# Performance work log

Measured on AMD Instinct MI355X. Metric: run time of the kernel, lower is better.

## Reference

```python
import jax, jax.numpy as jnp
import numpy as np

NEG_INF = -1e30


def setup_inputs() -> dict:
    key = jax.random.key(0)
    k1, k2, k3 = jax.random.split(key, 3)
    B, H, HKV, S, D = 2, 16, 4, 2048, 128
    q = jax.random.normal(k1, (B, H, S, D), dtype=jnp.float32)
    k = jax.random.normal(k2, (B, HKV, S, D), dtype=jnp.float32)
    v = jax.random.normal(k3, (B, HKV, S, D), dtype=jnp.float32)
    return {"q": q, "k": k, "v": v}


def reference(q, k, v):
    # Flash attention math (exact, non-tiled reference): causal + sliding-window
    # masked softmax(QK^T * scale) V with GQA head grouping.
    B, H, M, D = q.shape
    _, HKV, N, _ = k.shape
    G = H // HKV  # num_kv_groups
    W = 512       # sliding window size
    scale = 1.0 / jnp.sqrt(jnp.float32(D))

    qg = q.reshape(B, HKV, G, M, D)
    # scores: [B, HKV, G, M, N]
    scores = jnp.einsum("bkgmd,bknd->bkgmn", qg, k) * scale

    i = jnp.arange(M)[:, None]
    j = jnp.arange(N)[None, :]
    # causal: j <= i ; sliding window: only last W keys visible (i - j < W)
    keep = (j <= i) & ((i - j) < W)
    scores = jnp.where(keep[None, None, None], scores, NEG_INF)

    p = jax.nn.softmax(scores.astype(jnp.float32), axis=-1).astype(q.dtype)
    out = jnp.einsum("bkgmn,bknd->bkgmd", p, v)
    return out.reshape(B, H, M, D)
```

## Files before the change

kernel.cpp:

```cpp
#include <hip/hip_runtime.h>
#include <hip/hip_bf16.h>
#include <stdint.h>

#define SEQ 2048
#define HD  128
#define WIN 512
#define NH  16
#define NKV 4
#define BATCH 2

typedef __attribute__((ext_vector_type(8))) short bf16x8;
typedef __attribute__((ext_vector_type(4))) short bf16x4;
typedef __attribute__((ext_vector_type(4))) float f32x4;
typedef __attribute__((ext_vector_type(4))) uint32_t u32x4;
typedef __attribute__((ext_vector_type(2))) uint32_t u32x2;

#define EXP2(x) __builtin_amdgcn_exp2f(x)

#define AS1(p) ((const __attribute__((address_space(1))) uint32_t*)(p))
#define AS3(p) ((__attribute__((address_space(3))) uint32_t*)(p))

__device__ __forceinline__ uint32_t pk2(float a, float b) {
    __hip_bfloat162 h = __float22bfloat162_rn(make_float2(a, b));
    return *reinterpret_cast<uint32_t*>(&h);
}

__global__ __launch_bounds__(256) void prep_kv(
    const float* __restrict__ k,
    const float* __restrict__ v,
    uint16_t* __restrict__ kb,
    uint16_t* __restrict__ vt)
{
    const int tile = blockIdx.x;
    const int kvh  = tile >> 5;
    const int kt   = tile & 31;
    const int t    = threadIdx.x;

    const float* ksrc = k + ((size_t)kvh * SEQ + kt * 64) * HD;
    const float* vsrc = v + ((size_t)kvh * SEQ + kt * 64) * HD;
    uint16_t* kdst = kb + ((size_t)kvh * SEQ + kt * 64) * HD;
    uint16_t* vdst = vt + ((size_t)kvh * 32 + kt) * (size_t)(64 * HD);

    __shared__ uint16_t lv[64][132];

    #pragma unroll
    for (int i = 0; i < 8; ++i) {
        int u = t + i * 256;
        int row = u >> 5, c4 = u & 31;
        float4 f = *reinterpret_cast<const float4*>(vsrc + row * HD + c4 * 4);
        u32x2 w; w.x = pk2(f.x, f.y); w.y = pk2(f.z, f.w);
        *reinterpret_cast<u32x2*>(&lv[row][c4 * 4]) = w;
    }
    #pragma unroll
    for (int i = 0; i < 8; ++i) {
        int u = t + i * 256;
        int row = u >> 5, c4 = u & 31;
        float4 f = *reinterpret_cast<const float4*>(ksrc + row * HD + c4 * 4);
        u32x2 w; w.x = pk2(f.x, f.y); w.y = pk2(f.z, f.w);
        int col = c4 * 4;
        int e = row * HD + ((((col >> 3) ^ (row & 7)) << 3) | (col & 7));
        *reinterpret_cast<u32x2*>(&kdst[e]) = w;
    }
    __syncthreads();
    #pragma unroll
    for (int i = 0; i < 4; ++i) {
        int g = t + i * 256;
        int dim = g >> 3, pg = g & 7;
        uint32_t w[4];
        #pragma unroll
        for (int jj = 0; jj < 4; ++jj) {
            int p0 = pg * 8 + jj * 2;
            int s0 = p0 >> 5, w0 = p0 & 31;
            int key0 = s0 * 32 + ((w0 >> 2) & 1) * 16 + (w0 >> 3) * 4 + (w0 & 3);
            int p1 = p0 + 1;
            int s1 = p1 >> 5, w1 = p1 & 31;
            int key1 = s1 * 32 + ((w1 >> 2) & 1) * 16 + (w1 >> 3) * 4 + (w1 & 3);
            w[jj] = (uint32_t)lv[key0][dim] | ((uint32_t)lv[key1][dim] << 16);
        }
        int e = dim * 64 + ((pg ^ (dim & 7)) << 3);
        u32x4 wv = {w[0], w[1], w[2], w[3]};
        *reinterpret_cast<u32x4*>(&vdst[e]) = wv;
    }
}

__global__ __launch_bounds__(512, 2) void fa_mfma(
    const float* __restrict__ q,
    const uint16_t* __restrict__ kb,
    const uint16_t* __restrict__ vt,
    float* __restrict__ out)
{
    const int tid  = threadIdx.x;
    const int wave = tid >> 6;
    const int lane = tid & 63;
    const int l4   = lane >> 4;
    const int l15  = lane & 15;

    const int bh   = blockIdx.x >> 4;
    const int qblk = blockIdx.x & 15;
    const int q0   = qblk << 7;
    const int hkv  = (bh & (NH - 1)) >> 2;
    const int b    = bh >> 4;

    const int i0   = q0 + wave * 16;

    __shared__ __align__(16) uint16_t lds_k[2][64 * HD];
    __shared__ __align__(16) uint16_t lds_vt[2][64 * HD];

    const float scale2 = 0.08838834764831845f * 1.4426950408889634f;

    const size_t qbase = (size_t)bh * SEQ * HD;
    const uint16_t* kt_base = kb + (size_t)(b * NKV + hkv) * SEQ * HD;
    const uint16_t* vt_base = vt + (size_t)(b * NKV + hkv) * SEQ * HD;

    bf16x8 qf[4];
    {
        const float* qr = q + qbase + (size_t)(i0 + l15) * HD;
        #pragma unroll
        for (int ks = 0; ks < 4; ++ks) {
            const float4* g = reinterpret_cast<const float4*>(qr + ks * 32 + l4 * 8);
            float4 a = g[0], bq = g[1];
            u32x4 t;
            t.x = pk2(a.x * scale2, a.y * scale2);
            t.y = pk2(a.z * scale2, a.w * scale2);
            t.z = pk2(bq.x * scale2, bq.y * scale2);
            t.w = pk2(bq.z * scale2, bq.w * scale2);
            qf[ks] = __builtin_bit_cast(bf16x8, t);
        }
    }

    f32x4 O[8];
    #pragma unroll
    for (int a2 = 0; a2 < 8; ++a2) O[a2] = (f32x4){0.f, 0.f, 0.f, 0.f};
    float mrow = -1e30f;
    float lrow = 0.f;

    const int kt_lo_blk = (q0 >= 512) ? ((q0 - 511) >> 6) : 0;
    const int kt_hi_blk = (q0 + 127) >> 6;
    const int lo_w = (i0 >= 512) ? ((i0 - 511) >> 6) : 0;
    const int hi_w = (i0 + 15) >> 6;

    auto stage = [&](int kt, int pb) {
        const uint16_t* ks = kt_base + (size_t)kt * 64 * HD;
        const uint16_t* vs = vt_base + (size_t)kt * 64 * HD;
        const int ch = wave * 2;
        #pragma unroll
        for (int c = 0; c < 2; ++c) {
            __builtin_amdgcn_global_load_lds(
                AS1(ks + (ch + c) * 512 + lane * 8),
                AS3(&lds_k[pb][(ch + c) * 512]), 16, 0, 0);
            __builtin_amdgcn_global_load_lds(
                AS1(vs + (ch + c) * 512 + lane * 8),
                AS3(&lds_vt[pb][(ch + c) * 512]), 16, 0, 0);
        }
    };

    stage(kt_lo_blk, 0);
    __syncthreads();

    int par = 0;
    for (int kt = kt_lo_blk; kt <= kt_hi_blk; ++kt) {
        if (kt < kt_hi_blk) stage(kt + 1, par ^ 1);

        if (kt >= lo_w && kt <= hi_w) {
            f32x4 sf[4];
            #pragma unroll
            for (int mt = 0; mt < 4; ++mt) sf[mt] = (f32x4){0.f, 0.f, 0.f, 0.f};
            __builtin_amdgcn_s_setprio(1);
            #pragma unroll
            for (int mt = 0; mt < 4; ++mt) {
                const int arow = mt * 16 + l15;
                #pragma unroll
                for (int ks = 0; ks < 4; ++ks) {
                    bf16x8 af = *reinterpret_cast<const bf16x8*>(
                        &lds_k[par][arow * HD + ((((ks * 4 + l4) ^ (arow & 7))) << 3)]);
                    sf[mt] = __builtin_amdgcn_mfma_f32_16x16x32_bf16(
                        af, qf[ks], sf[mt], 0, 0, 0);
                }
            }
            __builtin_amdgcn_s_setprio(0);
            const bool needmask = (kt == hi_w) || (kt == lo_w && i0 > 511);
            if (needmask) {
                const int iq = i0 + l15;
                #pragma unroll
                for (int mt = 0; mt < 4; ++mt) {
                    int jb = kt * 64 + mt * 16 + l4 * 4;
                    #pragma unroll
                    for (int r = 0; r < 4; ++r) {
                        int j = jb + r;
                        if (!((j <= iq) && (iq - j < WIN))) sf[mt][r] = -1e30f;
                    }
                }
            }
            float a0 = fmaxf(fmaxf(sf[0][0], sf[0][1]), fmaxf(sf[0][2], sf[0][3]));
            float a1 = fmaxf(fmaxf(sf[1][0], sf[1][1]), fmaxf(sf[1][2], sf[1][3]));
            float a2 = fmaxf(fmaxf(sf[2][0], sf[2][1]), fmaxf(sf[2][2], sf[2][3]));
            float a3 = fmaxf(fmaxf(sf[3][0], sf[3][1]), fmaxf(sf[3][2], sf[3][3]));
            float tm = fmaxf(fmaxf(a0, a1), fmaxf(a2, a3));
            tm = fmaxf(tm, __shfl_xor(tm, 16, 64));
            tm = fmaxf(tm, __shfl_xor(tm, 32, 64));
            const bool defer = __all(tm <= mrow + 8.0f);
            if (!defer) {
                float mn = fmaxf(mrow, tm);
                float alpha = EXP2(mrow - mn);
                mrow = mn;
                lrow *= alpha;
                #pragma unroll
                for (int r = 0; r < 4; ++r) {
                    float ar = __shfl(alpha, l4 * 4 + r, 64);
                    #pragma unroll
                    for (int nt = 0; nt < 8; ++nt) O[nt][r] *= ar;
                }
            }
            bf16x4 pfrag[4];
            {
                float me = fmaxf(mrow, -1e20f);
                float s[4];
                #pragma unroll
                for (int mt = 0; mt < 4; ++mt) {
                    float p0 = EXP2(sf[mt][0] - me);
                    float p1 = EXP2(sf[mt][1] - me);
                    float p2 = EXP2(sf[mt][2] - me);
                    float p3 = EXP2(sf[mt][3] - me);
                    u32x2 t;
                    t.x = pk2(p0, p1);
                    t.y = pk2(p2, p3);
                    pfrag[mt] = __builtin_bit_cast(bf16x4, t);
                    s[mt] = (p0 + p1) + (p2 + p3);
                }
                float ts = (s[0] + s[1]) + (s[2] + s[3]);
                ts += __shfl_xor(ts, 16, 64);
                ts += __shfl_xor(ts, 32, 64);
                lrow += ts;
            }
            __builtin_amdgcn_s_setprio(1);
            #pragma unroll
            for (int s = 0; s < 2; ++s) {
                bf16x8 pa = __builtin_shufflevector(pfrag[2 * s], pfrag[2 * s + 1],
                                                    0, 1, 2, 3, 4, 5, 6, 7);
                #pragma unroll
                for (int nt = 0; nt < 8; ++nt) {
                    const int vr = nt * 16 + l15;
                    bf16x8 vf = *reinterpret_cast<const bf16x8*>(
                        &lds_vt[par][vr * 64 + ((((s * 4 + l4) ^ (vr & 7))) << 3)]);
                    O[nt] = __builtin_amdgcn_mfma_f32_16x16x32_bf16(pa, vf, O[nt], 0, 0, 0);
                }
            }
            __builtin_amdgcn_s_setprio(0);
        }
        __syncthreads();
        par ^= 1;
    }

    {
        float inv = 1.0f / lrow;
        #pragma unroll
        for (int r = 0; r < 4; ++r) {
            float li = __shfl(inv, l4 * 4 + r, 64);
            int row = i0 + l4 * 4 + r;
            float* orow = out + qbase + (size_t)row * HD;
            #pragma unroll
            for (int nt = 0; nt < 8; ++nt)
                orow[nt * 16 + l15] = O[nt][r] * li;
        }
    }
}

#define KSTR 136
#define VSTR 72
#define VT_ROWS (HD * VSTR + (HD / 4) * 4)
__device__ __forceinline__ int vt_off(int row, int col) {
    return row * VSTR + (row >> 2) * 4 + col;
}

__global__ __launch_bounds__(512, 2)
void fa_mfma_fused(
    const float* __restrict__ q,
    const float* __restrict__ k,
    const float* __restrict__ v,
    float* __restrict__ out)
{
    const int tid  = threadIdx.x;
    const int wave = tid >> 6;
    const int lane = tid & 63;
    const int l4   = lane >> 4;
    const int l15  = lane & 15;

    const int bh   = blockIdx.x >> 4;
    const int qblk = blockIdx.x & 15;
    const int q0   = qblk << 7;
    const int hkv  = (bh & (NH - 1)) >> 2;
    const int b    = bh >> 4;

    const int i0   = q0 + wave * 16;

    __shared__ __align__(16) uint16_t lds_k[2][64 * KSTR];
    __shared__ __align__(16) uint16_t lds_vt[2][VT_ROWS];

    const float scale2 = 0.08838834764831845f * 1.4426950408889634f;

    const size_t qbase  = (size_t)bh * SEQ * HD;
    const size_t kvbase = (size_t)(b * NKV + hkv) * SEQ * HD;

    bf16x8 qf[4];
    {
        const float* qr = q + qbase + (size_t)(i0 + l15) * HD;
        #pragma unroll
        for (int ks = 0; ks < 4; ++ks) {
            const float4* g = reinterpret_cast<const float4*>(qr + ks * 32 + l4 * 8);
            float4 a = g[0], bq = g[1];
            u32x4 t;
            t.x = pk2(a.x * scale2, a.y * scale2);
            t.y = pk2(a.z * scale2, a.w * scale2);
            t.z = pk2(bq.x * scale2, bq.y * scale2);
            t.w = pk2(bq.z * scale2, bq.w * scale2);
            qf[ks] = __builtin_bit_cast(bf16x8, t);
        }
    }

    f32x4 O[8];
    #pragma unroll
    for (int a2 = 0; a2 < 8; ++a2) O[a2] = (f32x4){0.f, 0.f, 0.f, 0.f};
    float mrow = -1e30f;
    float lrow = 0.f;

    const int kt_lo_blk = (q0 >= 512) ? ((q0 - 511) >> 6) : 0;
    const int kt_hi_blk = (q0 + 127) >> 6;
    const int lo_w = (i0 >= 512) ? ((i0 - 511) >> 6) : 0;
    const int hi_w = (i0 + 15) >> 6;

    const int vdg = tid & 31;
    const int vkg = tid >> 5;
    float4 rKa[2], rKb[2], rV[4];

    auto prefetch_k = [&](int kt) {
        const float* kp = k + kvbase + (size_t)kt * 64 * HD;
        #pragma unroll
        for (int it = 0; it < 2; ++it) {
            int flat8 = tid + it * 512, key = flat8 >> 4, ch = flat8 & 15;
            const float4* g = reinterpret_cast<const float4*>(kp + key * HD + ch * 8);
            rKa[it] = g[0]; rKb[it] = g[1];
        }
    };
    auto prefetch_v = [&](int kt) {
        const float* vp = v + kvbase + (size_t)kt * 64 * HD;
        #pragma unroll
        for (int r = 0; r < 4; ++r)
            rV[r] = *reinterpret_cast<const float4*>(vp + (vkg * 4 + r) * HD + vdg * 4);
    };
    auto pack_k = [&](int pb) {
        #pragma unroll
        for (int it = 0; it < 2; ++it) {
            int flat8 = tid + it * 512, key = flat8 >> 4, ch = flat8 & 15;
            uint4 wv;
            wv.x = pk2(rKa[it].x, rKa[it].y);  wv.y = pk2(rKa[it].z, rKa[it].w);
            wv.z = pk2(rKb[it].x, rKb[it].y);  wv.w = pk2(rKb[it].z, rKb[it].w);
            *reinterpret_cast<uint4*>(&lds_k[pb][key * KSTR + ch * 8]) = wv;
        }
    };
    auto pack_v = [&](int pb) {
        const float* rvf = reinterpret_cast<const float*>(rV);
        #pragma unroll
        for (int i = 0; i < 4; ++i) {
            u32x2 wv;
            wv.x = pk2(rvf[0 * 4 + i], rvf[1 * 4 + i]);
            wv.y = pk2(rvf[2 * 4 + i], rvf[3 * 4 + i]);
            *reinterpret_cast<u32x2*>(&lds_vt[pb][vt_off(vdg * 4 + i, vkg * 4)]) = wv;
        }
    };

    prefetch_k(kt_lo_blk);
    prefetch_v(kt_lo_blk);
    pack_k(0);
    pack_v(0);
    __syncthreads();

    int par = 0;
    for (int kt = kt_lo_blk; kt <= kt_hi_blk; ++kt) {
        const bool more = (kt < kt_hi_blk);
        if (more) prefetch_k(kt + 1);

        if (kt >= lo_w && kt <= hi_w) {
            f32x4 sf[4];
            #pragma unroll
            for (int mt = 0; mt < 4; ++mt) sf[mt] = (f32x4){0.f, 0.f, 0.f, 0.f};
            __builtin_amdgcn_s_setprio(1);
            #pragma unroll
            for (int mt = 0; mt < 4; ++mt) {
                #pragma unroll
                for (int ks = 0; ks < 4; ++ks) {
                    bf16x8 af = *reinterpret_cast<const bf16x8*>(
                        &lds_k[par][(mt * 16 + l15) * KSTR + ks * 32 + l4 * 8]);
                    sf[mt] = __builtin_amdgcn_mfma_f32_16x16x32_bf16(
                        af, qf[ks], sf[mt], 0, 0, 0);
                }
            }
            __builtin_amdgcn_s_setprio(0);
            if (more) { pack_k(par ^ 1); prefetch_v(kt + 1); }
            const bool needmask = (kt == hi_w) || (kt == lo_w && i0 > 511);
            if (needmask) {
                const int iq = i0 + l15;
                #pragma unroll
                for (int mt = 0; mt < 4; ++mt) {
                    int jb = kt * 64 + mt * 16 + l4 * 4;
                    #pragma unroll
                    for (int r = 0; r < 4; ++r) {
                        int j = jb + r;
                        if (!((j <= iq) && (iq - j < WIN))) sf[mt][r] = -1e30f;
                    }
                }
            }
            float a0 = fmaxf(fmaxf(sf[0][0], sf[0][1]), fmaxf(sf[0][2], sf[0][3]));
            float a1 = fmaxf(fmaxf(sf[1][0], sf[1][1]), fmaxf(sf[1][2], sf[1][3]));
            float a2 = fmaxf(fmaxf(sf[2][0], sf[2][1]), fmaxf(sf[2][2], sf[2][3]));
            float a3 = fmaxf(fmaxf(sf[3][0], sf[3][1]), fmaxf(sf[3][2], sf[3][3]));
            float tm = fmaxf(fmaxf(a0, a1), fmaxf(a2, a3));
            tm = fmaxf(tm, __shfl_xor(tm, 16, 64));
            tm = fmaxf(tm, __shfl_xor(tm, 32, 64));
            const bool defer = __all(tm <= mrow + 8.0f);
            if (!defer) {
                float mn = fmaxf(mrow, tm);
                float alpha = EXP2(mrow - mn);
                mrow = mn;
                lrow *= alpha;
                #pragma unroll
                for (int r = 0; r < 4; ++r) {
                    float ar = __shfl(alpha, l4 * 4 + r, 64);
                    #pragma unroll
                    for (int nt = 0; nt < 8; ++nt) O[nt][r] *= ar;
                }
            }
            bf16x4 pfrag[4];
            {
                float me = fmaxf(mrow, -1e20f);
                float s[4];
                #pragma unroll
                for (int mt = 0; mt < 4; ++mt) {
                    float p0 = EXP2(sf[mt][0] - me);
                    float p1 = EXP2(sf[mt][1] - me);
                    float p2 = EXP2(sf[mt][2] - me);
                    float p3 = EXP2(sf[mt][3] - me);
                    u32x2 t;
                    t.x = pk2(p0, p1);
                    t.y = pk2(p2, p3);
                    pfrag[mt] = __builtin_bit_cast(bf16x4, t);
                    s[mt] = (p0 + p1) + (p2 + p3);
                }
                float ts = (s[0] + s[1]) + (s[2] + s[3]);
                ts += __shfl_xor(ts, 16, 64);
                ts += __shfl_xor(ts, 32, 64);
                lrow += ts;
            }
            if (more) pack_v(par ^ 1);
            __builtin_amdgcn_s_setprio(1);
            #pragma unroll
            for (int s = 0; s < 2; ++s) {
                bf16x8 pa = __builtin_shufflevector(pfrag[2 * s], pfrag[2 * s + 1],
                                                    0, 1, 2, 3, 4, 5, 6, 7);
                #pragma unroll
                for (int nt = 0; nt < 8; ++nt) {
                    const int vr = nt * 16 + l15;
                    bf16x4 v0 = *reinterpret_cast<const bf16x4*>(
                        &lds_vt[par][vt_off(vr, s * 32 + l4 * 4)]);
                    bf16x4 v1 = *reinterpret_cast<const bf16x4*>(
                        &lds_vt[par][vt_off(vr, s * 32 + 16 + l4 * 4)]);
                    bf16x8 vf = __builtin_shufflevector(v0, v1, 0, 1, 2, 3, 4, 5, 6, 7);
                    O[nt] = __builtin_amdgcn_mfma_f32_16x16x32_bf16(pa, vf, O[nt], 0, 0, 0);
                }
            }
            __builtin_amdgcn_s_setprio(0);
        } else {
            if (more) { prefetch_v(kt + 1); pack_k(par ^ 1); pack_v(par ^ 1); }
        }
        __syncthreads();
        par ^= 1;
    }

    {
        float inv = 1.0f / lrow;
        #pragma unroll
        for (int r = 0; r < 4; ++r) {
            float li = __shfl(inv, l4 * 4 + r, 64);
            int row = i0 + l4 * 4 + r;
            float* orow = out + qbase + (size_t)row * HD;
            #pragma unroll
            for (int nt = 0; nt < 8; ++nt)
                orow[nt * 16 + l15] = O[nt][r] * li;
        }
    }
}

extern "C" void kernel_launch(void* const* d_in, const int* in_sizes, int n_in,
                              void* d_out, int out_size, void* d_ws, size_t ws_size,
                              hipStream_t stream) {
    const float* q = (const float*)d_in[0];
    const float* k = (const float*)d_in[1];
    const float* v = (const float*)d_in[2];
    float* out     = (float*)d_out;

    const size_t kv_elems = (size_t)BATCH * NKV * SEQ * HD;
    const size_t ws_needed = kv_elems * 2u * sizeof(uint16_t);

    if (d_ws != nullptr && ws_size >= ws_needed) {
        uint16_t* kb  = (uint16_t*)d_ws;
        uint16_t* vtw = kb + kv_elems;
        hipLaunchKernelGGL(prep_kv, dim3(BATCH * NKV * (SEQ / 64)), dim3(256), 0,
                           stream, k, v, kb, vtw);
        hipLaunchKernelGGL(fa_mfma, dim3(BATCH * NH * (SEQ / 128)), dim3(512), 0,
                           stream, q, kb, vtw, out);
    } else {
        hipLaunchKernelGGL(fa_mfma_fused, dim3(BATCH * NH * (SEQ / 128)), dim3(512),
                           0, stream, q, k, v, out);
    }
}
```

Baseline: 121.0 us.

## Enlarge attention tiles to 256 queries per block and 128-key KV tiles

After: 127.9 us. 1.06x slower.

```diff
diff --git a/kernel.cpp b/kernel.cpp
--- a/kernel.cpp
+++ b/kernel.cpp
@@ -83,7 +83,8 @@
     }
 }
 
-__global__ __launch_bounds__(512, 2) void fa_mfma(
+__global__ __launch_bounds__(512) __attribute__((amdgpu_waves_per_eu(2, 2)))
+void fa_mfma(
     const float* __restrict__ q,
     const uint16_t* __restrict__ kb,
     const uint16_t* __restrict__ vt,
@@ -95,6 +96,214 @@
     const int l4   = lane >> 4;
     const int l15  = lane & 15;
 
+    const int bh   = blockIdx.x >> 3;
+    const int qblk = blockIdx.x & 7;
+    const int q0   = qblk << 8;
+    const int hkv  = (bh & (NH - 1)) >> 2;
+    const int b    = bh >> 4;
+
+    const int i0   = q0 + wave * 32;
+
+    __shared__ __align__(16) uint16_t lds_k[2][128 * HD];
+    __shared__ __align__(16) uint16_t lds_vt[2][128 * HD];
+
+    const float scale2 = 0.08838834764831845f * 1.4426950408889634f;
+
+    const size_t qbase = (size_t)bh * SEQ * HD;
+    const uint16_t* kt_base = kb + (size_t)(b * NKV + hkv) * SEQ * HD;
+    const uint16_t* vt_base = vt + (size_t)(b * NKV + hkv) * SEQ * HD;
+
+    bf16x8 qf[2][4];
+    #pragma unroll
+    for (int sub = 0; sub < 2; ++sub) {
+        const float* qr = q + qbase + (size_t)(i0 + sub * 16 + l15) * HD;
+        #pragma unroll
+        for (int ks = 0; ks < 4; ++ks) {
+            const float4* g = reinterpret_cast<const float4*>(qr + ks * 32 + l4 * 8);
+            float4 a = g[0], bq = g[1];
+            u32x4 t;
+            t.x = pk2(a.x * scale2, a.y * scale2);
+            t.y = pk2(a.z * scale2, a.w * scale2);
+            t.z = pk2(bq.x * scale2, bq.y * scale2);
+            t.w = pk2(bq.z * scale2, bq.w * scale2);
+            qf[sub][ks] = __builtin_bit_cast(bf16x8, t);
+        }
+    }
+
+    f32x4 O[2][8];
+    #pragma unroll
+    for (int a1 = 0; a1 < 2; ++a1)
+        #pragma unroll
+        for (int a2 = 0; a2 < 8; ++a2) O[a1][a2] = (f32x4){0.f, 0.f, 0.f, 0.f};
+    float mrow[2] = {-1e30f, -1e30f};
+    float lrow[2] = {0.f, 0.f};
+
+    const int kt_lo_blk = (q0 >= 512) ? ((q0 - 511) >> 7) : 0;
+    const int kt_hi_blk = (q0 + 255) >> 7;
+    const int lo_w = (i0 >= 512) ? ((i0 - 511) >> 7) : 0;
+    const int hi_w = (i0 + 31) >> 7;
+
+    auto stage = [&](int kt, int pb) {
+        const uint16_t* ks = kt_base + (size_t)kt * 128 * HD;
+        const uint16_t* vs = vt_base + (size_t)kt * 128 * HD;
+        #pragma unroll
+        for (int c = 0; c < 4; ++c) {
+            const int off = c * 4096 + tid * 8;
+            __builtin_amdgcn_global_load_lds(AS1(ks + off), AS3(&lds_k[pb][off]),
+                                             16, 0, 0);
+            __builtin_amdgcn_global_load_lds(AS1(vs + off), AS3(&lds_vt[pb][off]),
+                                             16, 0, 0);
+        }
+    };
+
+    stage(kt_lo_blk, 0);
+    __syncthreads();
+
+    int par = 0;
+    for (int kt = kt_lo_blk; kt <= kt_hi_blk; ++kt) {
+        if (kt < kt_hi_blk) stage(kt + 1, par ^ 1);
+
+        if (kt >= lo_w && kt <= hi_w) {
+            f32x4 sf[2][8];
+            #pragma unroll
+            for (int sub = 0; sub < 2; ++sub)
+                #pragma unroll
+                for (int mt = 0; mt < 8; ++mt) sf[sub][mt] = (f32x4){0.f, 0.f, 0.f, 0.f};
+            __builtin_amdgcn_s_setprio(1);
+            #pragma unroll
+            for (int mt = 0; mt < 8; ++mt) {
+                const int arow = mt * 16 + l15;
+                #pragma unroll
+                for (int ks = 0; ks < 4; ++ks) {
+                    bf16x8 af = *reinterpret_cast<const bf16x8*>(
+                        &lds_k[par][arow * HD + ((((ks * 4 + l4) ^ (arow & 7))) << 3)]);
+                    sf[0][mt] = __builtin_amdgcn_mfma_f32_16x16x32_bf16(
+                        af, qf[0][ks], sf[0][mt], 0, 0, 0);
+                    sf[1][mt] = __builtin_amdgcn_mfma_f32_16x16x32_bf16(
+                        af, qf[1][ks], sf[1][mt], 0, 0, 0);
+                }
+            }
+            __builtin_amdgcn_s_setprio(0);
+            const bool needmask = (kt == hi_w) || (kt == lo_w && i0 >= 512);
+            if (needmask) {
+                #pragma unroll
+                for (int sub = 0; sub < 2; ++sub) {
+                    const int iq = i0 + sub * 16 + l15;
+                    #pragma unroll
+                    for (int mt = 0; mt < 8; ++mt) {
+                        int jb = kt * 128 + mt * 16 + l4 * 4;
+                        #pragma unroll
+                        for (int r = 0; r < 4; ++r) {
+                            int j = jb + r;
+                            if (!((j <= iq) && (iq - j < WIN))) sf[sub][mt][r] = -1e30f;
+                        }
+                    }
+                }
+            }
+            bf16x4 pfrag[2][8];
+            #pragma unroll
+            for (int sub = 0; sub < 2; ++sub) {
+                float tmx = -1e30f;
+                #pragma unroll
+                for (int mt = 0; mt < 8; ++mt) {
+                    float a = fmaxf(fmaxf(sf[sub][mt][0], sf[sub][mt][1]),
+                                    fmaxf(sf[sub][mt][2], sf[sub][mt][3]));
+                    tmx = fmaxf(tmx, a);
+                }
+                tmx = fmaxf(tmx, __shfl_xor(tmx, 16, 64));
+                tmx = fmaxf(tmx, __shfl_xor(tmx, 32, 64));
+                const bool defer = __all(tmx <= mrow[sub] + 8.0f);
+                if (!defer) {
+                    float mn = fmaxf(mrow[sub], tmx);
+                    float alpha = EXP2(mrow[sub] - mn);
+                    mrow[sub] = mn;
+                    lrow[sub] *= alpha;
+                    #pragma unroll
+                    for (int r = 0; r < 4; ++r) {
+                        float ar = __shfl(alpha, l4 * 4 + r, 64);
+                        #pragma unroll
+                        for (int nt = 0; nt < 8; ++nt) O[sub][nt][r] *= ar;
+                    }
+                }
+                float me = fmaxf(mrow[sub], -1e20f);
+                float ts = 0.f;
+                #pragma unroll
+                for (int mt = 0; mt < 8; ++mt) {
+                    float p0 = EXP2(sf[sub][mt][0] - me);
+                    float p1 = EXP2(sf[sub][mt][1] - me);
+                    float p2 = EXP2(sf[sub][mt][2] - me);
+                    float p3 = EXP2(sf[sub][mt][3] - me);
+                    u32x2 t;
+                    t.x = pk2(p0, p1);
+                    t.y = pk2(p2, p3);
+                    pfrag[sub][mt] = __builtin_bit_cast(bf16x4, t);
+                    ts += (p0 + p1) + (p2 + p3);
+                }
+                ts += __shfl_xor(ts, 16, 64);
+                ts += __shfl_xor(ts, 32, 64);
+                lrow[sub] += ts;
+            }
+            __builtin_amdgcn_s_setprio(1);
+            #pragma unroll
+            for (int s = 0; s < 4; ++s) {
+                const int st = s >> 1, s2 = s & 1;
+                bf16x8 pa0 = __builtin_shufflevector(pfrag[0][2 * s], pfrag[0][2 * s + 1],
+                                                     0, 1, 2, 3, 4, 5, 6, 7);
+                bf16x8 pa1 = __builtin_shufflevector(pfrag[1][2 * s], pfrag[1][2 * s + 1],
+                                                     0, 1, 2, 3, 4, 5, 6, 7);
+                #pragma unroll
+                for (int nt = 0; nt < 8; ++nt) {
+                    const int vr = nt * 16 + l15;
+                    bf16x8 vf = *reinterpret_cast<const bf16x8*>(
+                        &lds_vt[par][st * 8192 + vr * 64 +
+                                     ((((s2 * 4 + l4) ^ (vr & 7))) << 3)]);
+                    O[0][nt] = __builtin_amdgcn_mfma_f32_16x16x32_bf16(
+                        pa0, vf, O[0][nt], 0, 0, 0);
+                    O[1][nt] = __builtin_amdgcn_mfma_f32_16x16x32_bf16(
+                        pa1, vf, O[1][nt], 0, 0, 0);
+                }
+            }
+            __builtin_amdgcn_s_setprio(0);
+        }
+        __syncthreads();
+        par ^= 1;
+    }
+
+    #pragma unroll
+    for (int sub = 0; sub < 2; ++sub) {
+        float inv = 1.0f / lrow[sub];
+        #pragma unroll
+        for (int r = 0; r < 4; ++r) {
+            float li = __shfl(inv, l4 * 4 + r, 64);
+            int row = i0 + sub * 16 + l4 * 4 + r;
+            float* orow = out + qbase + (size_t)row * HD;
+            #pragma unroll
+            for (int nt = 0; nt < 8; ++nt)
+                orow[nt * 16 + l15] = O[sub][nt][r] * li;
+        }
+    }
+}
+
+#define KSTR 136
+#define VSTR 72
+#define VT_ROWS (HD * VSTR + (HD / 4) * 4)
+__device__ __forceinline__ int vt_off(int row, int col) {
+    return row * VSTR + (row >> 2) * 4 + col;
+}
+
+__global__ __launch_bounds__(512, 2)
+void fa_mfma_fused(
+    const float* __restrict__ q,
+    const float* __restrict__ k,
+    const float* __restrict__ v,
+    float* __restrict__ out)
+{
+    const int tid  = threadIdx.x;
+    const int wave = tid >> 6;
+    const int lane = tid & 63;
+    const int l4   = lane >> 4;
+    const int l15  = lane & 15;
+
     const int bh   = blockIdx.x >> 4;
     const int qblk = blockIdx.x & 15;
     const int q0   = qblk << 7;
@@ -103,14 +312,13 @@
 
     const int i0   = q0 + wave * 16;
 
-    __shared__ __align__(16) uint16_t lds_k[2][64 * HD];
-    __shared__ __align__(16) uint16_t lds_vt[2][64 * HD];
+    __shared__ __align__(16) uint16_t lds_k[2][64 * KSTR];
+    __shared__ __align__(16) uint16_t lds_vt[2][VT_ROWS];
 
     const float scale2 = 0.08838834764831845f * 1.4426950408889634f;
 
-    const size_t qbase = (size_t)bh * SEQ * HD;
-    const uint16_t* kt_base = kb + (size_t)(b * NKV + hkv) * SEQ * HD;
-    const uint16_t* vt_base = vt + (size_t)(b * NKV + hkv) * SEQ * HD;
+    const size_t qbase  = (size_t)bh * SEQ * HD;
+    const size_t kvbase = (size_t)(b * NKV + hkv) * SEQ * HD;
 
     bf16x8 qf[4];
     {
@@ -139,27 +347,56 @@
     const int lo_w = (i0 >= 512) ? ((i0 - 511) >> 6) : 0;
     const int hi_w = (i0 + 15) >> 6;
 
-    auto stage = [&](int kt, int pb) {
-        const uint16_t* ks = kt_base + (size_t)kt * 64 * HD;
-        const uint16_t* vs = vt_base + (size_t)kt * 64 * HD;
-        const int ch = wave * 2;
-        #pragma unroll
-        for (int c = 0; c < 2; ++c) {
-            __builtin_amdgcn_global_load_lds(
-                AS1(ks + (ch + c) * 512 + lane * 8),
-                AS3(&lds_k[pb][(ch + c) * 512]), 16, 0, 0);
-            __builtin_amdgcn_global_load_lds(
-                AS1(vs + (ch + c) * 512 + lane * 8),
-                AS3(&lds_vt[pb][(ch + c) * 512]), 16, 0, 0);
+    const int vdg = tid & 31;
+    const int vkg = tid >> 5;
+    float4 rKa[2], rKb[2], rV[4];
+
+    auto prefetch_k = [&](int kt) {
+        const float* kp = k + kvbase + (size_t)kt * 64 * HD;
+        #pragma unroll
+        for (int it = 0; it < 2; ++it) {
+            int flat8 = tid + it * 512, key = flat8 >> 4, ch = flat8 & 15;
+            const float4* g = reinterpret_cast<const float4*>(kp + key * HD + ch * 8);
+            rKa[it] = g[0]; rKb[it] = g[1];
         }
     };
-
-    stage(kt_lo_blk, 0);
+    auto prefetch_v = [&](int kt) {
+        const float* vp = v + kvbase + (size_t)kt * 64 * HD;
+        #pragma unroll
+        for (int r = 0; r < 4; ++r)
+            rV[r] = *reinterpret_cast<const float4*>(vp + (vkg * 4 + r) * HD + vdg * 4);
+    };
+    auto pack_k = [&](int pb) {
+        #pragma unroll
+        for (int it = 0; it < 2; ++it) {
+            int flat8 = tid + it * 512, key = flat8 >> 4, ch = flat8 & 15;
+            uint4 wv;
+            wv.x = pk2(rKa[it].x, rKa[it].y);  wv.y = pk2(rKa[it].z, rKa[it].w);
+            wv.z = pk2(rKb[it].x, rKb[it].y);  wv.w = pk2(rKb[it].z, rKb[it].w);
+            *reinterpret_cast<uint4*>(&lds_k[pb][key * KSTR + ch * 8]) = wv;
+        }
+    };
+    auto pack_v = [&](int pb) {
+        const float* rvf = reinterpret_cast<const float*>(rV);
+        #pragma unroll
+        for (int i = 0; i < 4; ++i) {
+            u32x2 wv;
+            wv.x = pk2(rvf[0 * 4 + i], rvf[1 * 4 + i]);
+            wv.y = pk2(rvf[2 * 4 + i], rvf[3 * 4 + i]);
+            *reinterpret_cast<u32x2*>(&lds_vt[pb][vt_off(vdg * 4 + i, vkg * 4)]) = wv;
+        }
+    };
+
+    prefetch_k(kt_lo_blk);
+    prefetch_v(kt_lo_blk);
+    pack_k(0);
+    pack_v(0);
     __syncthreads();
 
     int par = 0;
     for (int kt = kt_lo_blk; kt <= kt_hi_blk; ++kt) {
-        if (kt < kt_hi_blk) stage(kt + 1, par ^ 1);
+        const bool more = (kt < kt_hi_blk);
+        if (more) prefetch_k(kt + 1);
 
         if (kt >= lo_w && kt <= hi_w) {
             f32x4 sf[4];
@@ -168,16 +405,16 @@
             __builtin_amdgcn_s_setprio(1);
             #pragma unroll
             for (int mt = 0; mt < 4; ++mt) {
-                const int arow = mt * 16 + l15;
                 #pragma unroll
                 for (int ks = 0; ks < 4; ++ks) {
                     bf16x8 af = *reinterpret_cast<const bf16x8*>(
-                        &lds_k[par][arow * HD + ((((ks * 4 + l4) ^ (arow & 7))) << 3)]);
+                        &lds_k[par][(mt * 16 + l15) * KSTR + ks * 32 + l4 * 8]);
                     sf[mt] = __builtin_amdgcn_mfma_f32_16x16x32_bf16(
                         af, qf[ks], sf[mt], 0, 0, 0);
                 }
             }
             __builtin_amdgcn_s_setprio(0);
+            if (more) { pack_k(par ^ 1); prefetch_v(kt + 1); }
             const bool needmask = (kt == hi_w) || (kt == lo_w && i0 > 511);
             if (needmask) {
                 const int iq = i0 + l15;
@@ -232,224 +469,6 @@
                 ts += __shfl_xor(ts, 32, 64);
                 lrow += ts;
             }
-            __builtin_amdgcn_s_setprio(1);
-            #pragma unroll
-            for (int s = 0; s < 2; ++s) {
-                bf16x8 pa = __builtin_shufflevector(pfrag[2 * s], pfrag[2 * s + 1],
-                                                    0, 1, 2, 3, 4, 5, 6, 7);
-                #pragma unroll
-                for (int nt = 0; nt < 8; ++nt) {
-                    const int vr = nt * 16 + l15;
-                    bf16x8 vf = *reinterpret_cast<const bf16x8*>(
-                        &lds_vt[par][vr * 64 + ((((s * 4 + l4) ^ (vr & 7))) << 3)]);
-                    O[nt] = __builtin_amdgcn_mfma_f32_16x16x32_bf16(pa, vf, O[nt], 0, 0, 0);
-                }
-            }
-            __builtin_amdgcn_s_setprio(0);
-        }
-        __syncthreads();
-        par ^= 1;
-    }
-
-    {
-        float inv = 1.0f / lrow;
-        #pragma unroll
-        for (int r = 0; r < 4; ++r) {
-            float li = __shfl(inv, l4 * 4 + r, 64);
-            int row = i0 + l4 * 4 + r;
-            float* orow = out + qbase + (size_t)row * HD;
-            #pragma unroll
-            for (int nt = 0; nt < 8; ++nt)
-                orow[nt * 16 + l15] = O[nt][r] * li;
-        }
-    }
-}
-
-#define KSTR 136
-#define VSTR 72
-#define VT_ROWS (HD * VSTR + (HD / 4) * 4)
-__device__ __forceinline__ int vt_off(int row, int col) {
-    return row * VSTR + (row >> 2) * 4 + col;
-}
-
-__global__ __launch_bounds__(512, 2)
-void fa_mfma_fused(
-    const float* __restrict__ q,
-    const float* __restrict__ k,
-    const float* __restrict__ v,
-    float* __restrict__ out)
-{
-    const int tid  = threadIdx.x;
-    const int wave = tid >> 6;
-    const int lane = tid & 63;
-    const int l4   = lane >> 4;
-    const int l15  = lane & 15;
-
-    const int bh   = blockIdx.x >> 4;
-    const int qblk = blockIdx.x & 15;
-    const int q0   = qblk << 7;
-    const int hkv  = (bh & (NH - 1)) >> 2;
-    const int b    = bh >> 4;
-
-    const int i0   = q0 + wave * 16;
-
-    __shared__ __align__(16) uint16_t lds_k[2][64 * KSTR];
-    __shared__ __align__(16) uint16_t lds_vt[2][VT_ROWS];
-
-    const float scale2 = 0.08838834764831845f * 1.4426950408889634f;
-
-    const size_t qbase  = (size_t)bh * SEQ * HD;
-    const size_t kvbase = (size_t)(b * NKV + hkv) * SEQ * HD;
-
-    bf16x8 qf[4];
-    {
-        const float* qr = q + qbase + (size_t)(i0 + l15) * HD;
-        #pragma unroll
-        for (int ks = 0; ks < 4; ++ks) {
-            const float4* g = reinterpret_cast<const float4*>(qr + ks * 32 + l4 * 8);
-            float4 a = g[0], bq = g[1];
-            u32x4 t;
-            t.x = pk2(a.x * scale2, a.y * scale2);
-            t.y = pk2(a.z * scale2, a.w * scale2);
-            t.z = pk2(bq.x * scale2, bq.y * scale2);
-            t.w = pk2(bq.z * scale2, bq.w * scale2);
-            qf[ks] = __builtin_bit_cast(bf16x8, t);
-        }
-    }
-
-    f32x4 O[8];
-    #pragma unroll
-    for (int a2 = 0; a2 < 8; ++a2) O[a2] = (f32x4){0.f, 0.f, 0.f, 0.f};
-    float mrow = -1e30f;
-    float lrow = 0.f;
-
-    const int kt_lo_blk = (q0 >= 512) ? ((q0 - 511) >> 6) : 0;
-    const int kt_hi_blk = (q0 + 127) >> 6;
-    const int lo_w = (i0 >= 512) ? ((i0 - 511) >> 6) : 0;
-    const int hi_w = (i0 + 15) >> 6;
-
-    const int vdg = tid & 31;
-    const int vkg = tid >> 5;
-    float4 rKa[2], rKb[2], rV[4];
-
-    auto prefetch_k = [&](int kt) {
-        const float* kp = k + kvbase + (size_t)kt * 64 * HD;
-        #pragma unroll
-        for (int it = 0; it < 2; ++it) {
-            int flat8 = tid + it * 512, key = flat8 >> 4, ch = flat8 & 15;
-            const float4* g = reinterpret_cast<const float4*>(kp + key * HD + ch * 8);
-            rKa[it] = g[0]; rKb[it] = g[1];
-        }
-    };
-    auto prefetch_v = [&](int kt) {
-        const float* vp = v + kvbase + (size_t)kt * 64 * HD;
-        #pragma unroll
-        for (int r = 0; r < 4; ++r)
-            rV[r] = *reinterpret_cast<const float4*>(vp + (vkg * 4 + r) * HD + vdg * 4);
-    };
-    auto pack_k = [&](int pb) {
-        #pragma unroll
-        for (int it = 0; it < 2; ++it) {
-            int flat8 = tid + it * 512, key = flat8 >> 4, ch = flat8 & 15;
-            uint4 wv;
-            wv.x = pk2(rKa[it].x, rKa[it].y);  wv.y = pk2(rKa[it].z, rKa[it].w);
-            wv.z = pk2(rKb[it].x, rKb[it].y);  wv.w = pk2(rKb[it].z, rKb[it].w);
-            *reinterpret_cast<uint4*>(&lds_k[pb][key * KSTR + ch * 8]) = wv;
-        }
-    };
-    auto pack_v = [&](int pb) {
-        const float* rvf = reinterpret_cast<const float*>(rV);
-        #pragma unroll
-        for (int i = 0; i < 4; ++i) {
-            u32x2 wv;
-            wv.x = pk2(rvf[0 * 4 + i], rvf[1 * 4 + i]);
-            wv.y = pk2(rvf[2 * 4 + i], rvf[3 * 4 + i]);
-            *reinterpret_cast<u32x2*>(&lds_vt[pb][vt_off(vdg * 4 + i, vkg * 4)]) = wv;
-        }
-    };
-
-    prefetch_k(kt_lo_blk);
-    prefetch_v(kt_lo_blk);
-    pack_k(0);
-    pack_v(0);
-    __syncthreads();
-
-    int par = 0;
-    for (int kt = kt_lo_blk; kt <= kt_hi_blk; ++kt) {
-        const bool more = (kt < kt_hi_blk);
-        if (more) prefetch_k(kt + 1);
-
-        if (kt >= lo_w && kt <= hi_w) {
-            f32x4 sf[4];
-            #pragma unroll
-            for (int mt = 0; mt < 4; ++mt) sf[mt] = (f32x4){0.f, 0.f, 0.f, 0.f};
-            __builtin_amdgcn_s_setprio(1);
-            #pragma unroll
-            for (int mt = 0; mt < 4; ++mt) {
-                #pragma unroll
-                for (int ks = 0; ks < 4; ++ks) {
-                    bf16x8 af = *reinterpret_cast<const bf16x8*>(
-                        &lds_k[par][(mt * 16 + l15) * KSTR + ks * 32 + l4 * 8]);
-                    sf[mt] = __builtin_amdgcn_mfma_f32_16x16x32_bf16(
-                        af, qf[ks], sf[mt], 0, 0, 0);
-                }
-            }
-            __builtin_amdgcn_s_setprio(0);
-            if (more) { pack_k(par ^ 1); prefetch_v(kt + 1); }
-            const bool needmask = (kt == hi_w) || (kt == lo_w && i0 > 511);
-            if (needmask) {
-                const int iq = i0 + l15;
-                #pragma unroll
-                for (int mt = 0; mt < 4; ++mt) {
-                    int jb = kt * 64 + mt * 16 + l4 * 4;
-                    #pragma unroll
-                    for (int r = 0; r < 4; ++r) {
-                        int j = jb + r;
-                        if (!((j <= iq) && (iq - j < WIN))) sf[mt][r] = -1e30f;
-                    }
-                }
-            }
-            float a0 = fmaxf(fmaxf(sf[0][0], sf[0][1]), fmaxf(sf[0][2], sf[0][3]));
-            float a1 = fmaxf(fmaxf(sf[1][0], sf[1][1]), fmaxf(sf[1][2], sf[1][3]));
-            float a2 = fmaxf(fmaxf(sf[2][0], sf[2][1]), fmaxf(sf[2][2], sf[2][3]));
-            float a3 = fmaxf(fmaxf(sf[3][0], sf[3][1]), fmaxf(sf[3][2], sf[3][3]));
-            float tm = fmaxf(fmaxf(a0, a1), fmaxf(a2, a3));
-            tm = fmaxf(tm, __shfl_xor(tm, 16, 64));
-            tm = fmaxf(tm, __shfl_xor(tm, 32, 64));
-            const bool defer = __all(tm <= mrow + 8.0f);
-            if (!defer) {
-                float mn = fmaxf(mrow, tm);
-                float alpha = EXP2(mrow - mn);
-                mrow = mn;
-                lrow *= alpha;
-                #pragma unroll
-                for (int r = 0; r < 4; ++r) {
-                    float ar = __shfl(alpha, l4 * 4 + r, 64);
-                    #pragma unroll
-                    for (int nt = 0; nt < 8; ++nt) O[nt][r] *= ar;
-                }
-            }
-            bf16x4 pfrag[4];
-            {
-                float me = fmaxf(mrow, -1e20f);
-                float s[4];
-                #pragma unroll
-                for (int mt = 0; mt < 4; ++mt) {
-                    float p0 = EXP2(sf[mt][0] - me);
-                    float p1 = EXP2(sf[mt][1] - me);
-                    float p2 = EXP2(sf[mt][2] - me);
-                    float p3 = EXP2(sf[mt][3] - me);
-                    u32x2 t;
-                    t.x = pk2(p0, p1);
-                    t.y = pk2(p2, p3);
-                    pfrag[mt] = __builtin_bit_cast(bf16x4, t);
-                    s[mt] = (p0 + p1) + (p2 + p3);
-                }
-                float ts = (s[0] + s[1]) + (s[2] + s[3]);
-                ts += __shfl_xor(ts, 16, 64);
-                ts += __shfl_xor(ts, 32, 64);
-                lrow += ts;
-            }
             if (more) pack_v(par ^ 1);
             __builtin_amdgcn_s_setprio(1);
             #pragma unroll
@@ -505,7 +524,7 @@
         uint16_t* vtw = kb + kv_elems;
         hipLaunchKernelGGL(prep_kv, dim3(BATCH * NKV * (SEQ / 64)), dim3(256), 0,
                            stream, k, v, kb, vtw);
-        hipLaunchKernelGGL(fa_mfma, dim3(BATCH * NH * (SEQ / 128)), dim3(512), 0,
+        hipLaunchKernelGGL(fa_mfma, dim3(BATCH * NH * (SEQ / 256)), dim3(512), 0,
                            stream, q, kb, vtw, out);
     } else {
         hipLaunchKernelGGL(fa_mfma_fused, dim3(BATCH * NH * (SEQ / 128)), dim3(512),
```
